# Performance work log

Hardware: AMD Instinct MI355X
Metric: run time of the kernel (lower is better)

Reference implementation:

```python
import jax, jax.numpy as jnp
import numpy as np

DIM = 256
HID = int(DIM * 2.66)        # 680
CH = 2 * HID                 # 1360, TVConv channels
K = 3
K2 = K * K
HP, WP = 14, 14
POSI = 4
INTER = min(64, HID // 2)    # 64
EPS = 1e-5


def conv2d(x, w, pad):
    # x: (B, Cin, H, W), w: (Cout, Cin, kh, kw)
    return jax.lax.conv_general_dilated(
        x, w, window_strides=(1, 1), padding=[(pad, pad), (pad, pad)],
        dimension_numbers=("NCHW", "OIHW", "NCHW"))


def layernorm_chw(x, g, b):
    # torch nn.LayerNorm([C, H, W]): normalize over last 3 dims, affine (C,H,W)
    mu = jnp.mean(x, axis=(1, 2, 3), keepdims=True)
    var = jnp.var(x, axis=(1, 2, 3), keepdims=True)
    return (x - mu) * jax.lax.rsqrt(var + EPS) * g + b


def weight_layers(posi_map, w0, g0, b0, w1, g1, b1, w2, g2, b2, wf):
    h = jax.nn.relu(layernorm_chw(conv2d(posi_map, w0, 1), g0, b0))
    h = jax.nn.relu(layernorm_chw(conv2d(h, w1, 1), g1, b1))
    h = jax.nn.relu(layernorm_chw(conv2d(h, w2, 1), g2, b2))
    return conv2d(h, wf, 1)  # (1, CH*K2, HP, WP)


def tvconv(x, weight):
    # x: (B, CH, HP, WP); weight: (1, CH, K2, HP, WP)
    B, C, H, W = x.shape
    xp = jnp.pad(x, ((0, 0), (0, 0), (1, 1), (1, 1)))
    # unfold ordering: channel-major, kernel positions row-major -> axis=2
    patches = jnp.stack([xp[:, :, i:i + H, j:j + W]
                         for i in range(K) for j in range(K)], axis=2)
    return jnp.sum(weight * patches, axis=2)  # (B, CH, H, W)


def frfn_forward(x, W_in, posi_map, w0, g0, b0, w1, g1, b1, w2, g2, b2, wf, W_out):
    h = jnp.einsum('oc,bchw->bohw', W_in, x)                      # project_in (1x1)
    wgt = weight_layers(posi_map, w0, g0, b0, w1, g1, b1, w2, g2, b2, wf)
    wgt = wgt.reshape(1, CH, K2, HP, WP)
    h = tvconv(h, wgt)                                            # (B, CH, H, W)
    x1, x2 = h[:, :HID], h[:, HID:]
    h = jax.nn.gelu(x1, approximate=False) * x2
    return jnp.einsum('oc,bchw->bohw', W_out, h)                  # project_out (1x1)


def setup_inputs() -> dict:
    key = jax.random.key(0)
    ks = jax.random.split(key, 16)
    s = 0.02
    out_chans = CH * K2
    return {
        "x": jax.random.normal(ks[0], (64, DIM, HP, WP), jnp.float32),
        "W_in": jax.random.normal(ks[1], (CH, DIM), jnp.float32) * s,
        "posi_map": jnp.ones((1, POSI, HP, WP), jnp.float32),
        "w0": jax.random.normal(ks[2], (INTER, POSI, K, K), jnp.float32) * s,
        "g0": jnp.ones((INTER, HP, WP), jnp.float32),
        "b0": jnp.zeros((INTER, HP, WP), jnp.float32),
        "w1": jax.random.normal(ks[3], (INTER, INTER, K, K), jnp.float32) * s,
        "g1": jnp.ones((INTER, HP, WP), jnp.float32),
        "b1": jnp.zeros((INTER, HP, WP), jnp.float32),
        "w2": jax.random.normal(ks[4], (INTER, INTER, K, K), jnp.float32) * s,
        "g2": jnp.ones((INTER, HP, WP), jnp.float32),
        "b2": jnp.zeros((INTER, HP, WP), jnp.float32),
        "wf": jax.random.normal(ks[5], (out_chans, INTER, K, K), jnp.float32) * s,
        "W_out": jax.random.normal(ks[6], (DIM, HID), jnp.float32) * s,
    }


def reference(x, W_in, posi_map, w0, g0, b0, w1, g1, b1, w2, g2, b2, wf, W_out):
    return frfn_forward(x, W_in, posi_map, w0, g0, b0, w1, g1, b1, w2, g2, b2, wf, W_out)
```

## Files before the change

### kernel.cpp

```cpp
#include <hip/hip_runtime.h>
#include <math.h>

#define DIMC   256
#define HID    680
#define CHN    1360
#define HP     14
#define WP     14
#define P      196
#define POSI   4
#define INTER  64
#define BATCH  64
#define KPAD   704
#define OUTCH  12240
#define MW     1408
#define MTOT   12672
#define KIM    576
#define MPADIN 1408
#define EPSLN  1e-5f

typedef __attribute__((ext_vector_type(8))) short short8;
typedef __attribute__((ext_vector_type(4))) short short4v;
typedef __attribute__((ext_vector_type(4))) float f32x4;

#define OFS_WBIN  0u
#define OFS_WBOUT 720896u
#define OFS_XT    1081344u
#define OFS_V0    7503872u
#define OFS_V1    7554048u
#define OFS_V2    7604224u
#define OFS_WGTT  7654656u
#define OFS_H1T   12452736u
#define OFS_HGT   46580608u
#define OFS_IMC   64242560u
#define OFS_WFB   64468352u
#define OFS_PST   79066496u

__device__ __forceinline__ unsigned short f2bf(float f) {
    union { float f; unsigned u; } v; v.f = f;
    unsigned u = v.u;
    return (unsigned short)((u + 0x7FFFu + ((u >> 16) & 1u)) >> 16);
}
__device__ __forceinline__ float bf2f(unsigned short h) {
    union { unsigned u; float f; } v; v.u = ((unsigned)h) << 16; return v.f;
}

__device__ __forceinline__ void gl2lds16(const unsigned short* g, unsigned short* l) {
    __builtin_amdgcn_global_load_lds(
        (const __attribute__((address_space(1))) unsigned int*)g,
        (__attribute__((address_space(3))) unsigned int*)l, 16, 0, 0);
}
__device__ __forceinline__ short8 fragld64(const unsigned short* S, int row, int lp) {
    int slot = ((row >> 1) + lp) & 7;
    return *(const short8*)(S + row * 64 + slot * 8);
}

__device__ __forceinline__ void block_reduce2(float& s, float& ss, float* red, int tid, int nthreads) {
    #pragma unroll
    for (int off = 32; off > 0; off >>= 1) {
        s  += __shfl_down(s, off);
        ss += __shfl_down(ss, off);
    }
    int wid = tid >> 6, nw = nthreads >> 6;
    if ((tid & 63) == 0) { red[wid*2] = s; red[wid*2+1] = ss; }
    __syncthreads();
    if (tid == 0) {
        float S = 0.f, SS = 0.f;
        for (int i = 0; i < nw; i++) { S += red[i*2]; SS += red[i*2+1]; }
        red[0] = S; red[1] = SS;
    }
    __syncthreads();
    s = red[0]; ss = red[1];
}

__device__ __forceinline__ void sum_pstat(const float* __restrict__ pstat, int base,
                                          float& s, float& ss) {
    s = 0.f; ss = 0.f;
    #pragma unroll
    for (int i = 0; i < 49; i++) {
        s  += pstat[base + 2*i];
        ss += pstat[base + 2*i + 1];
    }
}

#define NWIN  (MPADIN*DIMC)
#define NWOUT (DIMC*KPAD)
#define XT0   49
#define WF0   561
#define C0    2343
#define IMZ0  2475
#define PRE_BLKS 2489

__global__ __launch_bounds__(256) void k_pre(const float* __restrict__ Win,
                                             const float* __restrict__ Wout,
                                             const float* __restrict__ x,
                                             const float* __restrict__ wf,
                                             const float* __restrict__ posi,
                                             const float* __restrict__ w0,
                                             unsigned short* __restrict__ Wbin,
                                             unsigned short* __restrict__ Wbout,
                                             unsigned short* __restrict__ Xt,
                                             unsigned short* __restrict__ wfb,
                                             unsigned short* __restrict__ imc,
                                             float* __restrict__ v0,
                                             float* __restrict__ pstat) {
    __shared__ __align__(16) float smem[6304];
    int bid = blockIdx.x, tid = threadIdx.x;
    if (bid < XT0) {
        float (*ppad)[16][16] = (float(*)[16][16])smem;
        float* red = smem + 1024;
        for (int i = tid; i < POSI * 256; i += 256) {
            int cc = i >> 8, r = i & 255, ly = r >> 4, lx = r & 15;
            float v = 0.f;
            if (ly >= 1 && ly <= HP && lx >= 1 && lx <= WP) v = posi[cc*P + (ly-1)*WP + (lx-1)];
            ppad[cc][ly][lx] = v;
        }
        __syncthreads();
        int gid = bid * 256 + tid;
        int c = gid / P, p = gid - c*P, y = p / WP, x2 = p - (p/WP)*WP;
        float v = 0.f;
        #pragma unroll
        for (int ci = 0; ci < POSI; ci++) {
            const float* wr = w0 + (c*POSI + ci)*9;
            v += wr[0]*ppad[ci][y  ][x2] + wr[1]*ppad[ci][y  ][x2+1] + wr[2]*ppad[ci][y  ][x2+2]
               + wr[3]*ppad[ci][y+1][x2] + wr[4]*ppad[ci][y+1][x2+1] + wr[5]*ppad[ci][y+1][x2+2]
               + wr[6]*ppad[ci][y+2][x2] + wr[7]*ppad[ci][y+2][x2+1] + wr[8]*ppad[ci][y+2][x2+2];
        }
        v0[gid] = v;
        float s = v, ss = v * v;
        block_reduce2(s, ss, red, tid, 256);
        if (tid == 0) { pstat[2*bid] = s; pstat[2*bid + 1] = ss; }
    } else if (bid < WF0) {
        int b2 = bid - XT0;
        int b = b2 >> 3, c0 = (b2 & 7) * 32;
        float (*xs)[197] = (float(*)[197])smem;
        for (int i = tid; i < 32 * P; i += 256) {
            int ci = i / P, pp = i - ci * P;
            xs[ci][pp] = x[((size_t)b * DIMC + c0 + ci) * P + pp];
        }
        __syncthreads();
        for (int j = tid; j < P * 32; j += 256) {
            int ci = j & 31, pp = j >> 5;
            Xt[((size_t)b * P + pp) * DIMC + c0 + ci] = f2bf(xs[ci][pp]);
        }
    } else if (bid < C0) {
        int base = (bid - WF0) * 1024;
        #pragma unroll
        for (int k2 = 0; k2 < 4; k2++) {
            int t = base + k2 * 256 + tid;
            int j = t * 4;
            int rowi = j / KIM, q = j - rowi * KIM;
            int kk = rowi / MW, ch = rowi - kk * MW;
            short4v sv = (short4v)0;
            if (ch < CHN) {
                float4 v = *(const float4*)(wf + ((size_t)(ch * 9 + kk)) * KIM + q);
                sv[0] = (short)f2bf(v.x); sv[1] = (short)f2bf(v.y);
                sv[2] = (short)f2bf(v.z); sv[3] = (short)f2bf(v.w);
            }
            *(short4v*)(wfb + j) = sv;
        }
    } else if (bid < IMZ0) {
        int base = (bid - C0) * 1024;
        #pragma unroll
        for (int k2 = 0; k2 < 4; k2++) {
            int t = base + k2 * 256 + tid;
            int i0 = t * 4;
            if (i0 < NWIN) {
                short4v sv = (short4v)0;
                if (i0 < CHN * DIMC) {
                    float4 v = *(const float4*)(Win + i0);
                    sv[0] = (short)f2bf(v.x); sv[1] = (short)f2bf(v.y);
                    sv[2] = (short)f2bf(v.z); sv[3] = (short)f2bf(v.w);
                }
                *(short4v*)(Wbin + i0) = sv;
            } else {
                int j0 = i0 - NWIN;
                int o = j0 / KPAD, k = j0 - o * KPAD;
                short4v sv = (short4v)0;
                if (k < HID) {
                    float4 v = *(const float4*)(Wout + o * HID + k);
                    sv[0] = (short)f2bf(v.x); sv[1] = (short)f2bf(v.y);
                    sv[2] = (short)f2bf(v.z); sv[3] = (short)f2bf(v.w);
                }
                *(short4v*)(Wbout + j0) = sv;
            }
        }
    } else {
        int base = (bid - IMZ0) * 1024;
        #pragma unroll
        for (int k2 = 0; k2 < 4; k2++) {
            int cc = base + k2 * 256 + tid;
            if (cc < (P * KIM) / 8) *(short8*)(imc + cc * 8) = (short8)0;
        }
    }
}

__global__ __launch_bounds__(256) void k_convln(const float* __restrict__ v_in,
                                                const float* __restrict__ g,
                                                const float* __restrict__ b,
                                                const float* __restrict__ w,
                                                float* __restrict__ v_out,
                                                float* __restrict__ pstat,
                                                int psi, int pso) {
    __shared__ __align__(16) float as[INTER][16][16];
    __shared__ __align__(16) float wl[3][INTER][12];
    __shared__ float red[16];
    const float inv = 1.f / (float)(INTER * P);
    int tid = threadIdx.x;
    float s0, ss0;
    sum_pstat(pstat, psi, s0, ss0);
    float mu = s0 * inv;
    float var = ss0 * inv - mu * mu;
    float rstd = rsqrtf(var + EPSLN);

    int gid0 = blockIdx.x * 256;
    int cA = gid0 / P;
    for (int i = tid; i < 3 * INTER * 9; i += 256) {
        int cc = i / (INTER * 9), rest = i - cc * (INTER * 9);
        int ci = rest / 9, kk = rest - ci * 9;
        int crow = cA + cc; if (crow >= INTER) crow = INTER - 1;
        wl[cc][ci][kk] = w[(crow * INTER + ci) * 9 + kk];
    }
    for (int i = tid; i < INTER * 64; i += 256)
        *(f32x4*)((float*)as + i * 4) = (f32x4)0.f;
    __syncthreads();
    #pragma unroll
    for (int it = 0; it < 13; it++) {
        int q4 = it * 256 + tid;
        if (q4 < (INTER * P) / 4) {
            float4 vv = *(const float4*)(v_in + q4 * 4);
            float4 gg = *(const float4*)(g + q4 * 4);
            float4 bb = *(const float4*)(b + q4 * 4);
            float va[4] = {vv.x, vv.y, vv.z, vv.w};
            float ga[4] = {gg.x, gg.y, gg.z, gg.w};
            float ba[4] = {bb.x, bb.y, bb.z, bb.w};
            #pragma unroll
            for (int e = 0; e < 4; e++) {
                int idx = q4 * 4 + e;
                int ci = idx / P, p = idx - ci * P;
                int yy = p / WP, xx = p - yy * WP;
                float a = (va[e] - mu) * rstd * ga[e] + ba[e];
                as[ci][yy + 1][xx + 1] = a > 0.f ? a : 0.f;
            }
        }
    }
    __syncthreads();
    int gid = gid0 + tid;
    int c = gid / P, p = gid - c * P, y = p / WP, x = p - (p / WP) * WP;
    const float* wr0 = &wl[c - cA][0][0];
    float v = 0.f;
    for (int ci = 0; ci < INTER; ci++) {
        const float* wi = wr0 + ci * 12;
        v += wi[0]*as[ci][y  ][x] + wi[1]*as[ci][y  ][x+1] + wi[2]*as[ci][y  ][x+2]
           + wi[3]*as[ci][y+1][x] + wi[4]*as[ci][y+1][x+1] + wi[5]*as[ci][y+1][x+2]
           + wi[6]*as[ci][y+2][x] + wi[7]*as[ci][y+2][x+1] + wi[8]*as[ci][y+2][x+2];
    }
    v_out[gid] = v;
    float s = v, ss = v * v;
    block_reduce2(s, ss, red, tid, 256);
    if (tid == 0) { pstat[pso + 2*blockIdx.x] = s; pstat[pso + 2*blockIdx.x + 1] = ss; }
}

__global__ __launch_bounds__(256) void k_lnsc(const float* __restrict__ v_in,
                                              const float* __restrict__ g,
                                              const float* __restrict__ b,
                                              const float* __restrict__ pstat,
                                              unsigned short* __restrict__ imc) {
    const float inv = 1.f / (float)(INTER * P);
    int gid = blockIdx.x * 256 + threadIdx.x;
    float s0, ss0;
    sum_pstat(pstat, 196, s0, ss0);
    float mu = s0 * inv;
    float var = ss0 * inv - mu * mu;
    float rstd = rsqrtf(var + EPSLN);
    float a = (v_in[gid] - mu) * rstd * g[gid] + b[gid];
    a = a > 0.f ? a : 0.f;
    unsigned short bv = f2bf(a);
    int ci = gid / P, p = gid - ci * P, y = p / WP, x = p - (p / WP) * WP;
    #pragma unroll
    for (int k = 0; k < 9; k++) {
        int yp = y - (k / 3 - 1), xp = x - (k % 3 - 1);
        if (yp >= 0 && yp < HP && xp >= 0 && xp < WP)
            imc[(yp * WP + xp) * KIM + ci * 9 + k] = bv;
    }
}

__global__ __launch_bounds__(256) void k_gemm_wf(const unsigned short* __restrict__ wfb,
                                                 const unsigned short* __restrict__ imc,
                                                 unsigned short* __restrict__ wgtT) {
    __shared__ __align__(16) unsigned short buf[64*64 + 208*64];
    unsigned short* As = buf;
    unsigned short* Bs = buf + 64*64;
    unsigned short* ot = buf;
    int tid = threadIdx.x;
    int w = tid >> 6, lane = tid & 63, quad = lane >> 4, c16 = lane & 15;
    int m0 = blockIdx.x * 64;
    int kk = m0 / MW, ch0 = m0 - kk * MW;
    for (int i = tid; i < 96; i += 256)
        *(short8*)(Bs + 196 * 64 + i * 8) = (short8)0;
    f32x4 acc[13];
    #pragma unroll
    for (int f = 0; f < 13; f++) acc[f] = (f32x4)0.f;

    for (int kc = 0; kc < 9; ++kc) {
        int k0 = kc * 64;
        if (kc) __syncthreads();
        #pragma unroll
        for (int i = tid; i < 512; i += 256) {
            int r = i >> 3, s = i & 7, q = (s - (r >> 1)) & 7;
            gl2lds16(wfb + ((size_t)(kk * MW + ch0 + r)) * KIM + k0 + q * 8, As + (i & ~63) * 8);
        }
        for (int i = tid; i < 1568; i += 256) {
            int r = i >> 3, s = i & 7, q = (s - (r >> 1)) & 7;
            gl2lds16(imc + (size_t)r * KIM + k0 + q * 8, Bs + (i & ~63) * 8);
        }
        __syncthreads();
        #pragma unroll
        for (int ks = 0; ks < 2; ++ks) {
            short8 af = fragld64(As, w * 16 + c16, ks * 4 + quad);
            #pragma unroll
            for (int f = 0; f < 13; f++) {
                short8 bf = fragld64(Bs, f * 16 + c16, ks * 4 + quad);
                acc[f] = __builtin_amdgcn_mfma_f32_16x16x32_bf16(af, bf, acc[f], 0, 0, 0);
            }
        }
    }
    __syncthreads();
    #pragma unroll
    for (int f = 0; f < 13; f++) {
        int p = f * 16 + c16;
        if (p < P) {
            short4v sv;
            sv[0] = (short)f2bf(acc[f][0]);
            sv[1] = (short)f2bf(acc[f][1]);
            sv[2] = (short)f2bf(acc[f][2]);
            sv[3] = (short)f2bf(acc[f][3]);
            *(short4v*)(ot + p * 72 + w * 16 + quad * 4) = sv;
        }
    }
    __syncthreads();
    int nvalid = CHN - ch0; if (nvalid > 64) nvalid = 64;
    for (int p = tid; p < P; p += 256) {
        const short8* src = (const short8*)(ot + p * 72);
        unsigned short* dst = wgtT + ((size_t)p * 9 + kk) * CHN + ch0;
        #pragma unroll
        for (int j = 0; j < 8; j++)
            if (j * 8 < nvalid) *(short8*)(dst + j * 8) = src[j];
    }
}

__global__ __launch_bounds__(256) void k_gemm_in(const unsigned short* __restrict__ A,
                                                 const unsigned short* __restrict__ B,
                                                 unsigned short* __restrict__ C) {
    __shared__ __align__(16) unsigned short As[128 * 64];
    __shared__ __align__(16) unsigned short Bs[128 * 64];
    int tid = threadIdx.x;
    int w = tid >> 6, lane = tid & 63, quad = lane >> 4, c16 = lane & 15;
    int m0 = blockIdx.x * 128, n0 = blockIdx.y * 128;
    int wm = (w & 1) * 64, wn = (w >> 1) * 64;
    f32x4 acc[4][4];
    #pragma unroll
    for (int i = 0; i < 4; i++)
        #pragma unroll
        for (int j = 0; j < 4; j++) acc[i][j] = (f32x4)0.f;

    for (int kc = 0; kc < 4; ++kc) {
        int k0 = kc * 64;
        if (kc) __syncthreads();
        #pragma unroll
        for (int i = tid; i < 1024; i += 256) {
            int r = i >> 3, s = i & 7, q = (s - (r >> 1)) & 7;
            gl2lds16(A + (size_t)(m0 + r) * DIMC + k0 + q * 8, As + (i & ~63) * 8);
        }
        #pragma unroll
        for (int i = tid; i < 1024; i += 256) {
            int r = i >> 3, s = i & 7, q = (s - (r >> 1)) & 7;
            gl2lds16(B + (size_t)(n0 + r) * DIMC + k0 + q * 8, Bs + (i & ~63) * 8);
        }
        __syncthreads();
        #pragma unroll
        for (int ks = 0; ks < 2; ++ks) {
            short8 af[4], bfr[4];
            #pragma unroll
            for (int i = 0; i < 4; i++) af[i] = fragld64(As, wm + i * 16 + c16, ks * 4 + quad);
            #pragma unroll
            for (int j = 0; j < 4; j++) bfr[j] = fragld64(Bs, wn + j * 16 + c16, ks * 4 + quad);
            #pragma unroll
            for (int i = 0; i < 4; i++)
                #pragma unroll
                for (int j = 0; j < 4; j++)
                    acc[i][j] = __builtin_amdgcn_mfma_f32_16x16x32_bf16(af[i], bfr[j], acc[i][j], 0, 0, 0);
        }
    }
    #pragma unroll
    for (int j = 0; j < 4; j++) {
        int n = n0 + wn + j * 16 + c16;
        unsigned short* dst = C + (size_t)n * CHN;
        #pragma unroll
        for (int i = 0; i < 4; i++) {
            int m = m0 + wm + i * 16 + quad * 4;
            if (m < CHN) {
                short4v sv;
                sv[0] = (short)f2bf(acc[i][j][0]);
                sv[1] = (short)f2bf(acc[i][j][1]);
                sv[2] = (short)f2bf(acc[i][j][2]);
                sv[3] = (short)f2bf(acc[i][j][3]);
                *(short4v*)(dst + m) = sv;
            }
        }
    }
}

__global__ __launch_bounds__(256) void k_tvg(const unsigned short* __restrict__ h1t,
                                             const unsigned short* __restrict__ wgtT,
                                             unsigned short* __restrict__ hgt) {
    __shared__ __align__(16) unsigned short wl[9 * CHN];
    int id = blockIdx.x;
    int xcd = id & 7, q = id >> 3;
    int p = xcd * 25 + (q % 25);
    int bg = q / 25;
    if (p >= P) return;
    int b0 = bg * 16, tid = threadIdx.x;
    const unsigned short* wrow = wgtT + (size_t)p * 9 * CHN;
    for (int i = tid * 8; i < 9 * CHN; i += 256 * 8)
        *(short8*)(wl + i) = *(const short8*)(wrow + i);
    int y = p / WP, x = p - (p / WP) * WP;
    int pn[9]; bool pv[9];
    #pragma unroll
    for (int k = 0; k < 9; k++) {
        int yy = y + k / 3 - 1, xx = x + (k % 3) - 1;
        pv[k] = (yy >= 0 && yy < HP && xx >= 0 && xx < WP);
        pn[k] = pv[k] ? yy * WP + xx : 0;
    }
    __syncthreads();
    for (int j = tid; j < 16 * 85; j += 256) {
        int bl = j / 85, c = (j - bl * 85) * 8;
        int b = b0 + bl;
        const unsigned short* hb = h1t + (size_t)b * P * CHN;
        float s1[8], s2[8];
        #pragma unroll
        for (int e = 0; e < 8; e++) { s1[e] = 0.f; s2[e] = 0.f; }
        #pragma unroll
        for (int k = 0; k < 9; k++) {
            if (!pv[k]) continue;
            const unsigned short* hr = hb + (size_t)pn[k] * CHN + c;
            short8 h1v = *(const short8*)hr;
            short8 h2v = *(const short8*)(hr + HID);
            short8 w1v = *(const short8*)(wl + k * CHN + c);
            short8 w2v = *(const short8*)(wl + k * CHN + HID + c);
            #pragma unroll
            for (int e = 0; e < 8; e++) {
                s1[e] += bf2f((unsigned short)w1v[e]) * bf2f((unsigned short)h1v[e]);
                s2[e] += bf2f((unsigned short)w2v[e]) * bf2f((unsigned short)h2v[e]);
            }
        }
        short8 o;
        #pragma unroll
        for (int e = 0; e < 8; e++) {
            float gl = 0.5f * s1[e] * (1.f + erff(s1[e] * 0.70710678118654752f));
            o[e] = (short)f2bf(gl * s2[e]);
        }
        *(short8*)(hgt + ((size_t)b * P + p) * KPAD + c) = o;
    }
    if (tid < 48) {
        int bl = tid / 3, z = (tid - bl * 3) * 8;
        *(short8*)(hgt + ((size_t)(b0 + bl) * P + p) * KPAD + HID + z) = (short8)0;
    }
}

__global__ __launch_bounds__(256) void k_gemm_out(const unsigned short* __restrict__ A,
                                                  const unsigned short* __restrict__ B,
                                                  float* __restrict__ out) {
    __shared__ __align__(16) unsigned short As[64 * 64];
    __shared__ __align__(16) unsigned short Bs[128 * 64];
    int tid = threadIdx.x;
    int w = tid >> 6, lane = tid & 63, quad = lane >> 4, c16 = lane & 15;
    int m0 = blockIdx.x * 64, n0 = blockIdx.y * 128;
    int wm = (w & 1) * 32, wn = (w >> 1) * 64;
    f32x4 acc[2][4];
    #pragma unroll
    for (int i = 0; i < 2; i++)
        #pragma unroll
        for (int j = 0; j < 4; j++) acc[i][j] = (f32x4)0.f;

    for (int kc = 0; kc < 11; ++kc) {
        int k0 = kc * 64;
        if (kc) __syncthreads();
        #pragma unroll
        for (int i = tid; i < 512; i += 256) {
            int r = i >> 3, s = i & 7, q = (s - (r >> 1)) & 7;
            gl2lds16(A + (size_t)(m0 + r) * KPAD + k0 + q * 8, As + (i & ~63) * 8);
        }
        #pragma unroll
        for (int i = tid; i < 1024; i += 256) {
            int r = i >> 3, s = i & 7, q = (s - (r >> 1)) & 7;
            gl2lds16(B + (size_t)(n0 + r) * KPAD + k0 + q * 8, Bs + (i & ~63) * 8);
        }
        __syncthreads();
        #pragma unroll
        for (int ks = 0; ks < 2; ++ks) {
            short8 af[2], bfr[4];
            #pragma unroll
            for (int i = 0; i < 2; i++) af[i] = fragld64(As, wm + i * 16 + c16, ks * 4 + quad);
            #pragma unroll
            for (int j = 0; j < 4; j++) bfr[j] = fragld64(Bs, wn + j * 16 + c16, ks * 4 + quad);
            #pragma unroll
            for (int i = 0; i < 2; i++)
                #pragma unroll
                for (int j = 0; j < 4; j++)
                    acc[i][j] = __builtin_amdgcn_mfma_f32_16x16x32_bf16(af[i], bfr[j], acc[i][j], 0, 0, 0);
        }
    }
    #pragma unroll
    for (int j = 0; j < 4; j++) {
        int n = n0 + wn + j * 16 + c16;
        int b = n / P, pp = n - b * P;
        #pragma unroll
        for (int i = 0; i < 2; i++) {
            int m = m0 + wm + i * 16 + quad * 4;
            #pragma unroll
            for (int r = 0; r < 4; r++)
                out[((size_t)b * DIMC + m + r) * P + pp] = acc[i][j][r];
        }
    }
}

extern "C" void kernel_launch(void* const* d_in, const int* in_sizes, int n_in,
                              void* d_out, int out_size, void* d_ws, size_t ws_size,
                              hipStream_t stream) {
    (void)in_sizes; (void)n_in; (void)out_size; (void)ws_size;
    const float* x     = (const float*)d_in[0];
    const float* W_in  = (const float*)d_in[1];
    const float* posi  = (const float*)d_in[2];
    const float* w0    = (const float*)d_in[3];
    const float* g0    = (const float*)d_in[4];
    const float* b0    = (const float*)d_in[5];
    const float* w1    = (const float*)d_in[6];
    const float* g1    = (const float*)d_in[7];
    const float* b1    = (const float*)d_in[8];
    const float* w2    = (const float*)d_in[9];
    const float* g2    = (const float*)d_in[10];
    const float* b2    = (const float*)d_in[11];
    const float* wf    = (const float*)d_in[12];
    const float* W_out = (const float*)d_in[13];
    float* out = (float*)d_out;
    char* ws = (char*)d_ws;

    unsigned short* Wbin  = (unsigned short*)(ws + OFS_WBIN);
    unsigned short* Wbout = (unsigned short*)(ws + OFS_WBOUT);
    unsigned short* Xt    = (unsigned short*)(ws + OFS_XT);
    float*          v0    = (float*)(ws + OFS_V0);
    float*          v1    = (float*)(ws + OFS_V1);
    float*          v2    = (float*)(ws + OFS_V2);
    float*          pstat = (float*)(ws + OFS_PST);
    unsigned short* wgtT  = (unsigned short*)(ws + OFS_WGTT);
    unsigned short* h1t   = (unsigned short*)(ws + OFS_H1T);
    unsigned short* hgt   = (unsigned short*)(ws + OFS_HGT);
    unsigned short* imc   = (unsigned short*)(ws + OFS_IMC);
    unsigned short* wfb   = (unsigned short*)(ws + OFS_WFB);

    k_pre<<<PRE_BLKS, 256, 0, stream>>>(
        W_in, W_out, x, wf, posi, w0, Wbin, Wbout, Xt, wfb, imc, v0, pstat);
    k_convln<<<49, 256, 0, stream>>>(v0, g0, b0, w1, v1, pstat, 0, 98);
    k_convln<<<49, 256, 0, stream>>>(v1, g1, b1, w2, v2, pstat, 98, 196);
    k_lnsc  <<<49, 256, 0, stream>>>(v2, g2, b2, pstat, imc);
    k_gemm_wf<<<MTOT/64, 256, 0, stream>>>(wfb, imc, wgtT);
    k_gemm_in <<<dim3(MPADIN/128, (BATCH*P)/128), 256, 0, stream>>>(Wbin, Xt, h1t);
    k_tvg     <<<800, 256, 0, stream>>>(h1t, wgtT, hgt);
    k_gemm_out<<<dim3(DIMC/64, (BATCH*P)/128), 256, 0, stream>>>(Wbout, hgt, out);
}
```

Before: 231.2 us.

## Fuse small LN-conv stages with slices of input GEMM to fill idle CUs

The tiny weight-generation kernels (two conv+LN stages, the LN scatter, and the wf GEMM) each launched only 49–198 blocks and left most CUs idle. They are now merged into four combined launches, and each launch also runs a slice of the independent project-in GEMM tiles in its spare blocks, so that GEMM overlaps with the serial chain. The tvconv kernel is also split into twice as many blocks with 8 batches each instead of 16. Risks: dynamic LDS is sized for the larger of the two roles, which may lower occupancy, and the GEMM tiles must add up exactly to cover every tile.

```diff
diff --git a/kernel.cpp b/kernel.cpp
--- a/kernel.cpp
+++ b/kernel.cpp
@@ -194,34 +194,35 @@
     }
 }
 
-__global__ __launch_bounds__(256) void k_convln(const float* __restrict__ v_in,
-                                                const float* __restrict__ g,
-                                                const float* __restrict__ b,
-                                                const float* __restrict__ w,
-                                                float* __restrict__ v_out,
-                                                float* __restrict__ pstat,
-                                                int psi, int pso) {
-    __shared__ __align__(16) float as[INTER][16][16];
-    __shared__ __align__(16) float wl[3][INTER][12];
-    __shared__ float red[16];
+
+__device__ __forceinline__ void dev_convln(char* sm, int bid, int tid,
+                                           const float* __restrict__ v_in,
+                                           const float* __restrict__ g,
+                                           const float* __restrict__ b,
+                                           const float* __restrict__ w,
+                                           float* __restrict__ v_out,
+                                           float* __restrict__ pstat,
+                                           int psi, int pso) {
+    float* asf = (float*)sm;
+    float* wlf = asf + INTER * 256;
+    float* red = wlf + 3 * INTER * 12;
     const float inv = 1.f / (float)(INTER * P);
-    int tid = threadIdx.x;
     float s0, ss0;
     sum_pstat(pstat, psi, s0, ss0);
     float mu = s0 * inv;
     float var = ss0 * inv - mu * mu;
     float rstd = rsqrtf(var + EPSLN);
 
-    int gid0 = blockIdx.x * 256;
+    int gid0 = bid * 256;
     int cA = gid0 / P;
     for (int i = tid; i < 3 * INTER * 9; i += 256) {
         int cc = i / (INTER * 9), rest = i - cc * (INTER * 9);
         int ci = rest / 9, kk = rest - ci * 9;
         int crow = cA + cc; if (crow >= INTER) crow = INTER - 1;
-        wl[cc][ci][kk] = w[(crow * INTER + ci) * 9 + kk];
+        wlf[cc * (INTER * 12) + ci * 12 + kk] = w[(crow * INTER + ci) * 9 + kk];
     }
     for (int i = tid; i < INTER * 64; i += 256)
-        *(f32x4*)((float*)as + i * 4) = (f32x4)0.f;
+        *(f32x4*)(asf + i * 4) = (f32x4)0.f;
     __syncthreads();
     #pragma unroll
     for (int it = 0; it < 13; it++) {
@@ -239,34 +240,36 @@
                 int ci = idx / P, p = idx - ci * P;
                 int yy = p / WP, xx = p - yy * WP;
                 float a = (va[e] - mu) * rstd * ga[e] + ba[e];
-                as[ci][yy + 1][xx + 1] = a > 0.f ? a : 0.f;
+                asf[ci * 256 + (yy + 1) * 16 + (xx + 1)] = a > 0.f ? a : 0.f;
             }
         }
     }
     __syncthreads();
     int gid = gid0 + tid;
     int c = gid / P, p = gid - c * P, y = p / WP, x = p - (p / WP) * WP;
-    const float* wr0 = &wl[c - cA][0][0];
+    const float* wr0 = wlf + (c - cA) * (INTER * 12);
     float v = 0.f;
     for (int ci = 0; ci < INTER; ci++) {
         const float* wi = wr0 + ci * 12;
-        v += wi[0]*as[ci][y  ][x] + wi[1]*as[ci][y  ][x+1] + wi[2]*as[ci][y  ][x+2]
-           + wi[3]*as[ci][y+1][x] + wi[4]*as[ci][y+1][x+1] + wi[5]*as[ci][y+1][x+2]
-           + wi[6]*as[ci][y+2][x] + wi[7]*as[ci][y+2][x+1] + wi[8]*as[ci][y+2][x+2];
+        const float* a0 = asf + ci * 256 + y * 16 + x;
+        v += wi[0]*a0[0]  + wi[1]*a0[1]  + wi[2]*a0[2]
+           + wi[3]*a0[16] + wi[4]*a0[17] + wi[5]*a0[18]
+           + wi[6]*a0[32] + wi[7]*a0[33] + wi[8]*a0[34];
     }
     v_out[gid] = v;
     float s = v, ss = v * v;
     block_reduce2(s, ss, red, tid, 256);
-    if (tid == 0) { pstat[pso + 2*blockIdx.x] = s; pstat[pso + 2*blockIdx.x + 1] = ss; }
-}
-
-__global__ __launch_bounds__(256) void k_lnsc(const float* __restrict__ v_in,
-                                              const float* __restrict__ g,
-                                              const float* __restrict__ b,
-                                              const float* __restrict__ pstat,
-                                              unsigned short* __restrict__ imc) {
+    if (tid == 0) { pstat[pso + 2*bid] = s; pstat[pso + 2*bid + 1] = ss; }
+}
+
+__device__ __forceinline__ void dev_lnsc(int bid, int tid,
+                                         const float* __restrict__ v_in,
+                                         const float* __restrict__ g,
+                                         const float* __restrict__ b,
+                                         const float* __restrict__ pstat,
+                                         unsigned short* __restrict__ imc) {
     const float inv = 1.f / (float)(INTER * P);
-    int gid = blockIdx.x * 256 + threadIdx.x;
+    int gid = bid * 256 + tid;
     float s0, ss0;
     sum_pstat(pstat, 196, s0, ss0);
     float mu = s0 * inv;
@@ -284,78 +287,14 @@
     }
 }
 
-__global__ __launch_bounds__(256) void k_gemm_wf(const unsigned short* __restrict__ wfb,
-                                                 const unsigned short* __restrict__ imc,
-                                                 unsigned short* __restrict__ wgtT) {
-    __shared__ __align__(16) unsigned short buf[64*64 + 208*64];
-    unsigned short* As = buf;
-    unsigned short* Bs = buf + 64*64;
-    unsigned short* ot = buf;
-    int tid = threadIdx.x;
+__device__ __forceinline__ void dev_gemm_in(char* sm, int mb, int nb, int tid,
+                                            const unsigned short* __restrict__ A,
+                                            const unsigned short* __restrict__ B,
+                                            unsigned short* __restrict__ C) {
+    unsigned short* As = (unsigned short*)sm;
+    unsigned short* Bs = As + 128 * 64;
     int w = tid >> 6, lane = tid & 63, quad = lane >> 4, c16 = lane & 15;
-    int m0 = blockIdx.x * 64;
-    int kk = m0 / MW, ch0 = m0 - kk * MW;
-    for (int i = tid; i < 96; i += 256)
-        *(short8*)(Bs + 196 * 64 + i * 8) = (short8)0;
-    f32x4 acc[13];
-    #pragma unroll
-    for (int f = 0; f < 13; f++) acc[f] = (f32x4)0.f;
-
-    for (int kc = 0; kc < 9; ++kc) {
-        int k0 = kc * 64;
-        if (kc) __syncthreads();
-        #pragma unroll
-        for (int i = tid; i < 512; i += 256) {
-            int r = i >> 3, s = i & 7, q = (s - (r >> 1)) & 7;
-            gl2lds16(wfb + ((size_t)(kk * MW + ch0 + r)) * KIM + k0 + q * 8, As + (i & ~63) * 8);
-        }
-        for (int i = tid; i < 1568; i += 256) {
-            int r = i >> 3, s = i & 7, q = (s - (r >> 1)) & 7;
-            gl2lds16(imc + (size_t)r * KIM + k0 + q * 8, Bs + (i & ~63) * 8);
-        }
-        __syncthreads();
-        #pragma unroll
-        for (int ks = 0; ks < 2; ++ks) {
-            short8 af = fragld64(As, w * 16 + c16, ks * 4 + quad);
-            #pragma unroll
-            for (int f = 0; f < 13; f++) {
-                short8 bf = fragld64(Bs, f * 16 + c16, ks * 4 + quad);
-                acc[f] = __builtin_amdgcn_mfma_f32_16x16x32_bf16(af, bf, acc[f], 0, 0, 0);
-            }
-        }
-    }
-    __syncthreads();
-    #pragma unroll
-    for (int f = 0; f < 13; f++) {
-        int p = f * 16 + c16;
-        if (p < P) {
-            short4v sv;
-            sv[0] = (short)f2bf(acc[f][0]);
-            sv[1] = (short)f2bf(acc[f][1]);
-            sv[2] = (short)f2bf(acc[f][2]);
-            sv[3] = (short)f2bf(acc[f][3]);
-            *(short4v*)(ot + p * 72 + w * 16 + quad * 4) = sv;
-        }
-    }
-    __syncthreads();
-    int nvalid = CHN - ch0; if (nvalid > 64) nvalid = 64;
-    for (int p = tid; p < P; p += 256) {
-        const short8* src = (const short8*)(ot + p * 72);
-        unsigned short* dst = wgtT + ((size_t)p * 9 + kk) * CHN + ch0;
-        #pragma unroll
-        for (int j = 0; j < 8; j++)
-            if (j * 8 < nvalid) *(short8*)(dst + j * 8) = src[j];
-    }
-}
-
-__global__ __launch_bounds__(256) void k_gemm_in(const unsigned short* __restrict__ A,
-                                                 const unsigned short* __restrict__ B,
-                                                 unsigned short* __restrict__ C) {
-    __shared__ __align__(16) unsigned short As[128 * 64];
-    __shared__ __align__(16) unsigned short Bs[128 * 64];
-    int tid = threadIdx.x;
-    int w = tid >> 6, lane = tid & 63, quad = lane >> 4, c16 = lane & 15;
-    int m0 = blockIdx.x * 128, n0 = blockIdx.y * 128;
+    int m0 = mb * 128, n0 = nb * 128;
     int wm = (w & 1) * 64, wn = (w >> 1) * 64;
     f32x4 acc[4][4];
     #pragma unroll
@@ -410,6 +349,117 @@
     }
 }
 
+__device__ __forceinline__ void dev_gemm_wf(char* sm, int bid, int tid,
+                                            const unsigned short* __restrict__ wfb,
+                                            const unsigned short* __restrict__ imc,
+                                            unsigned short* __restrict__ wgtT) {
+    unsigned short* buf = (unsigned short*)sm;
+    unsigned short* As = buf;
+    unsigned short* Bs = buf + 64 * 64;
+    unsigned short* ot = buf;
+    int w = tid >> 6, lane = tid & 63, quad = lane >> 4, c16 = lane & 15;
+    int m0 = bid * 64;
+    int kk = m0 / MW, ch0 = m0 - kk * MW;
+    for (int i = tid; i < 96; i += 256)
+        *(short8*)(Bs + 196 * 64 + i * 8) = (short8)0;
+    f32x4 acc[13];
+    #pragma unroll
+    for (int f = 0; f < 13; f++) acc[f] = (f32x4)0.f;
+
+    for (int kc = 0; kc < 9; ++kc) {
+        int k0 = kc * 64;
+        if (kc) __syncthreads();
+        #pragma unroll
+        for (int i = tid; i < 512; i += 256) {
+            int r = i >> 3, s = i & 7, q = (s - (r >> 1)) & 7;
+            gl2lds16(wfb + ((size_t)(kk * MW + ch0 + r)) * KIM + k0 + q * 8, As + (i & ~63) * 8);
+        }
+        for (int i = tid; i < 1568; i += 256) {
+            int r = i >> 3, s = i & 7, q = (s - (r >> 1)) & 7;
+            gl2lds16(imc + (size_t)r * KIM + k0 + q * 8, Bs + (i & ~63) * 8);
+        }
+        __syncthreads();
+        #pragma unroll
+        for (int ks = 0; ks < 2; ++ks) {
+            short8 af = fragld64(As, w * 16 + c16, ks * 4 + quad);
+            #pragma unroll
+            for (int f = 0; f < 13; f++) {
+                short8 bf = fragld64(Bs, f * 16 + c16, ks * 4 + quad);
+                acc[f] = __builtin_amdgcn_mfma_f32_16x16x32_bf16(af, bf, acc[f], 0, 0, 0);
+            }
+        }
+    }
+    __syncthreads();
+    #pragma unroll
+    for (int f = 0; f < 13; f++) {
+        int p = f * 16 + c16;
+        if (p < P) {
+            short4v sv;
+            sv[0] = (short)f2bf(acc[f][0]);
+            sv[1] = (short)f2bf(acc[f][1]);
+            sv[2] = (short)f2bf(acc[f][2]);
+            sv[3] = (short)f2bf(acc[f][3]);
+            *(short4v*)(ot + p * 72 + w * 16 + quad * 4) = sv;
+        }
+    }
+    __syncthreads();
+    int nvalid = CHN - ch0; if (nvalid > 64) nvalid = 64;
+    for (int p = tid; p < P; p += 256) {
+        const short8* src = (const short8*)(ot + p * 72);
+        unsigned short* dst = wgtT + ((size_t)p * 9 + kk) * CHN + ch0;
+        #pragma unroll
+        for (int j = 0; j < 8; j++)
+            if (j * 8 < nvalid) *(short8*)(dst + j * 8) = src[j];
+    }
+}
+
+#define SLICE 210
+#define CONVLN_LDS ((INTER*256 + 3*INTER*12 + 16) * 4)
+#define GEMMWF_LDS ((64*64 + 208*64) * 2)
+
+extern __shared__ char dynsm[];
+
+__global__ __launch_bounds__(256) void k_mA(const float* v0, const float* g0,
+                                            const float* b0, const float* w1,
+                                            float* v1, float* pstat,
+                                            const unsigned short* Wbin,
+                                            const unsigned short* Xt,
+                                            unsigned short* h1t) {
+    int bid = blockIdx.x, tid = threadIdx.x;
+    if (bid < 49) dev_convln(dynsm, bid, tid, v0, g0, b0, w1, v1, pstat, 0, 98);
+    else { int fid = bid - 49; dev_gemm_in(dynsm, fid % 11, fid / 11, tid, Wbin, Xt, h1t); }
+}
+__global__ __launch_bounds__(256) void k_mB(const float* v1, const float* g1,
+                                            const float* b1, const float* w2,
+                                            float* v2, float* pstat,
+                                            const unsigned short* Wbin,
+                                            const unsigned short* Xt,
+                                            unsigned short* h1t) {
+    int bid = blockIdx.x, tid = threadIdx.x;
+    if (bid < 49) dev_convln(dynsm, bid, tid, v1, g1, b1, w2, v2, pstat, 98, 196);
+    else { int fid = SLICE + bid - 49; dev_gemm_in(dynsm, fid % 11, fid / 11, tid, Wbin, Xt, h1t); }
+}
+__global__ __launch_bounds__(256) void k_mC(const float* v2, const float* g2,
+                                            const float* b2, const float* pstat,
+                                            unsigned short* imc,
+                                            const unsigned short* Wbin,
+                                            const unsigned short* Xt,
+                                            unsigned short* h1t) {
+    int bid = blockIdx.x, tid = threadIdx.x;
+    if (bid < 49) dev_lnsc(bid, tid, v2, g2, b2, pstat, imc);
+    else { int fid = 2 * SLICE + bid - 49; dev_gemm_in(dynsm, fid % 11, fid / 11, tid, Wbin, Xt, h1t); }
+}
+__global__ __launch_bounds__(256) void k_mD(const unsigned short* wfb,
+                                            const unsigned short* imc,
+                                            unsigned short* wgtT,
+                                            const unsigned short* Wbin,
+                                            const unsigned short* Xt,
+                                            unsigned short* h1t) {
+    int bid = blockIdx.x, tid = threadIdx.x;
+    if (bid < 198) dev_gemm_wf(dynsm, bid, tid, wfb, imc, wgtT);
+    else { int fid = 3 * SLICE + bid - 198; dev_gemm_in(dynsm, fid % 11, fid / 11, tid, Wbin, Xt, h1t); }
+}
+
 __global__ __launch_bounds__(256) void k_tvg(const unsigned short* __restrict__ h1t,
                                              const unsigned short* __restrict__ wgtT,
                                              unsigned short* __restrict__ hgt) {
@@ -419,7 +469,7 @@
     int p = xcd * 25 + (q % 25);
     int bg = q / 25;
     if (p >= P) return;
-    int b0 = bg * 16, tid = threadIdx.x;
+    int b0 = bg * 8, tid = threadIdx.x;
     const unsigned short* wrow = wgtT + (size_t)p * 9 * CHN;
     for (int i = tid * 8; i < 9 * CHN; i += 256 * 8)
         *(short8*)(wl + i) = *(const short8*)(wrow + i);
@@ -432,7 +482,7 @@
         pn[k] = pv[k] ? yy * WP + xx : 0;
     }
     __syncthreads();
-    for (int j = tid; j < 16 * 85; j += 256) {
+    for (int j = tid; j < 8 * 85; j += 256) {
         int bl = j / 85, c = (j - bl * 85) * 8;
         int b = b0 + bl;
         const unsigned short* hb = h1t + (size_t)b * P * CHN;
@@ -461,7 +511,7 @@
         }
         *(short8*)(hgt + ((size_t)b * P + p) * KPAD + c) = o;
     }
-    if (tid < 48) {
+    if (tid < 24) {
         int bl = tid / 3, z = (tid - bl * 3) * 8;
         *(short8*)(hgt + ((size_t)(b0 + bl) * P + p) * KPAD + HID + z) = (short8)0;
     }
@@ -560,11 +610,10 @@
 
     k_pre<<<PRE_BLKS, 256, 0, stream>>>(
         W_in, W_out, x, wf, posi, w0, Wbin, Wbout, Xt, wfb, imc, v0, pstat);
-    k_convln<<<49, 256, 0, stream>>>(v0, g0, b0, w1, v1, pstat, 0, 98);
-    k_convln<<<49, 256, 0, stream>>>(v1, g1, b1, w2, v2, pstat, 98, 196);
-    k_lnsc  <<<49, 256, 0, stream>>>(v2, g2, b2, pstat, imc);
-    k_gemm_wf<<<MTOT/64, 256, 0, stream>>>(wfb, imc, wgtT);
-    k_gemm_in <<<dim3(MPADIN/128, (BATCH*P)/128), 256, 0, stream>>>(Wbin, Xt, h1t);
-    k_tvg     <<<800, 256, 0, stream>>>(h1t, wgtT, hgt);
+    k_mA<<<49 + SLICE, 256, CONVLN_LDS, stream>>>(v0, g0, b0, w1, v1, pstat, Wbin, Xt, h1t);
+    k_mB<<<49 + SLICE, 256, CONVLN_LDS, stream>>>(v1, g1, b1, w2, v2, pstat, Wbin, Xt, h1t);
+    k_mC<<<49 + SLICE, 256, CONVLN_LDS, stream>>>(v2, g2, b2, pstat, imc, Wbin, Xt, h1t);
+    k_mD<<<198 + 448, 256, GEMMWF_LDS, stream>>>(wfb, imc, wgtT, Wbin, Xt, h1t);
+    k_tvg     <<<1600, 256, 0, stream>>>(h1t, wgtT, hgt);
     k_gemm_out<<<dim3(DIMC/64, (BATCH*P)/128), 256, 0, stream>>>(Wbout, hgt, out);
 }
```

Measured after the change: 217.9 us. 1.06x faster.
